# Optimization experiments

Measured on AMD Instinct MI355X. Metric: run time of the kernel, lower is better.

Reference implementation:

```python
import jax, jax.numpy as jnp
import numpy as np

B, L, H, NH = 8, 384, 512, 8
DH = H // NH
MAX_SEQ_LEN = 384


def setup_inputs() -> dict:
    key = jax.random.key(0)
    ks = jax.random.split(key, 16)
    s = 0.02
    seq_len = jnp.concatenate([
        jnp.array([L], dtype=jnp.int32),
        jax.random.randint(ks[3], (B - 1,), L // 2, L + 1, dtype=jnp.int32),
    ])
    return {
        "key": jax.random.normal(ks[0], (B, L, H), jnp.float32),
        "query": jax.random.normal(ks[1], (B, L, H), jnp.float32),
        "value": jax.random.normal(ks[2], (B, L, H), jnp.float32),
        "seq_len": seq_len,
        "pe": jax.random.normal(ks[4], (2 * MAX_SEQ_LEN + 1, H), jnp.float32) * s,
        "Wk": jax.random.normal(ks[5], (H, H), jnp.float32) * s,
        "bk": jnp.zeros((H,), jnp.float32),
        "Wq": jax.random.normal(ks[6], (H, H), jnp.float32) * s,
        "bq": jnp.zeros((H,), jnp.float32),
        "Wv": jax.random.normal(ks[7], (H, H), jnp.float32) * s,
        "bv": jnp.zeros((H,), jnp.float32),
        "Wr": jax.random.normal(ks[8], (H, H), jnp.float32) * s,
        "br": jnp.zeros((H,), jnp.float32),
        "u_bias": jax.random.normal(ks[9], (NH, DH), jnp.float32) * s,
        "v_bias": jax.random.normal(ks[10], (NH, DH), jnp.float32) * s,
        "Wff": jax.random.normal(ks[11], (H, H), jnp.float32) * s,
        "bff": jnp.zeros((H,), jnp.float32),
    }


def reference(key, query, value, seq_len, pe, Wk, bk, Wq, bq, Wv, bv, Wr, br, u_bias, v_bias, Wff, bff):
    # relative distances: rel[i, j] = j - i, in [-(L-1), L-1]
    rel = jnp.arange(L)[None, :] - jnp.arange(L)[:, None]          # [L, L]
    rpe = pe[rel + MAX_SEQ_LEN]                                    # [L, L, H]

    k = (key @ Wk.T + bk).reshape(B, L, NH, DH)
    q = (query @ Wq.T + bq).reshape(B, L, NH, DH)
    v = (value @ Wv.T + bv).reshape(B, L, NH, DH)
    rpe = (rpe @ Wr.T + br).reshape(L, L, NH, DH)

    # Transformer-XL score terms
    A = jnp.einsum('bihd,bjhd->bhij', q, k)                        # content-content
    Bt = jnp.einsum('bihd,ijhd->bhij', q, rpe)                     # content-position
    C = jnp.einsum('hd,bjhd->bhj', u_bias, k)[:, :, None, :]       # global content bias
    Dt = jnp.einsum('hd,ijhd->hij', v_bias, rpe)[None]             # global position bias

    scores = (A + Bt + C + Dt) / jnp.sqrt(jnp.float32(DH))
    key_mask = jnp.arange(L)[None, :] < seq_len[:, None]           # [B, L]
    scores = jnp.where(key_mask[:, None, None, :], scores, -1e15)
    attn = jax.nn.softmax(scores, axis=-1)                         # [B, NH, L, L]

    out = jnp.einsum('bhij,bjhd->bihd', attn, v).reshape(B, L, H)
    return out @ Wff.T + bff
```

## Files before the change

kernel.cpp:

```cpp
#include <hip/hip_runtime.h>

#define B_  8
#define L_  384
#define H_  512
#define NH_ 8
#define DH_ 64
#define RRM 768

typedef short bf16x8 __attribute__((ext_vector_type(8)));
typedef float f32x4  __attribute__((ext_vector_type(4)));
typedef unsigned int u32;
typedef u32 u32x4 __attribute__((ext_vector_type(4)));
#define MFMA_BF16 __builtin_amdgcn_mfma_f32_16x16x32_bf16

static __device__ __forceinline__ unsigned short f2bf(float f) {
    unsigned u = __builtin_bit_cast(unsigned, f);
    u += 0x7fffu + ((u >> 16) & 1u);
    return (unsigned short)(u >> 16);
}
static __device__ __forceinline__ float bf2f(unsigned short s) {
    unsigned u = ((unsigned)s) << 16;
    return __builtin_bit_cast(float, u);
}
static __device__ __forceinline__ u32 pk2(float lo, float hi) {
    u32 r;
    asm("v_cvt_pk_bf16_f32 %0, %1, %2" : "=v"(r) : "v"(lo), "v"(hi));
    return r;
}
static __device__ __forceinline__ void glds16(const void* g, void* l) {
    __builtin_amdgcn_global_load_lds(
        (const __attribute__((address_space(1))) u32*)g,
        (__attribute__((address_space(3))) u32*)l, 16, 0, 0);
}

struct WCvtArgs { const float* src[5]; unsigned short* dst[5]; };
__global__ __launch_bounds__(256) void cvt_w(WCvtArgs a) {
    const int gid = blockIdx.x * 256 + threadIdx.x;
    const int m = gid >> 15;
    const int rem = gid & 32767;
    const int row = rem >> 6, c = rem & 63;
    const int kc = c >> 3, sjd = c & 7;
    const int sjs = sjd ^ (row & 7);
    const float* s = a.src[m] + row * 512 + kc * 64 + sjs * 8;
    const f32x4 v0 = *(const f32x4*)s;
    const f32x4 v1 = *(const f32x4*)(s + 4);
    u32x4 o;
    o[0] = pk2(v0[0], v0[1]);
    o[1] = pk2(v0[2], v0[3]);
    o[2] = pk2(v1[0], v1[1]);
    o[3] = pk2(v1[2], v1[3]);
    *(u32x4*)(a.dst[m] + row * 512 + kc * 64 + sjd * 8) = o;
}

template <bool IS_FF>
__global__ __launch_bounds__(256) void gemm_nt(
    const float* __restrict__ A0, const float* __restrict__ A1,
    const float* __restrict__ A2, const float* __restrict__ A3,
    const unsigned short* __restrict__ Abf,
    const unsigned short* __restrict__ W0, const unsigned short* __restrict__ W1,
    const unsigned short* __restrict__ W2, const unsigned short* __restrict__ W3,
    const unsigned short* __restrict__ W4,
    const float* __restrict__ b0, const float* __restrict__ b1,
    const float* __restrict__ b2, const float* __restrict__ b3,
    const float* __restrict__ b4,
    const float* __restrict__ ub, const float* __restrict__ vbias,
    unsigned short* __restrict__ qu, unsigned short* __restrict__ qv,
    unsigned short* __restrict__ kb, unsigned short* __restrict__ vT,
    unsigned short* __restrict__ rp, float* __restrict__ ff) {

    const int z = IS_FF ? 4 : blockIdx.z;
    if (!IS_FF && z == 3 && blockIdx.y >= 12) return;
    const float* Af   = z == 0 ? A0 : z == 1 ? A1 : z == 2 ? A2 : A3;
    const unsigned short* Wb =
        z == 0 ? W0 : z == 1 ? W1 : z == 2 ? W2 : z == 3 ? W3 : W4;
    const float* bias = z == 0 ? b0 : z == 1 ? b1 : z == 2 ? b2 : z == 3 ? b3 : b4;

    __shared__ __align__(16) unsigned short AsF[2 * 64 * 64];
    __shared__ __align__(16) unsigned short BsF[2 * 128 * 64];

    const int tid = threadIdx.x;
    const int w = tid >> 6, lane = tid & 63;
    const int quad = lane >> 4, lm = lane & 15;
    const int wr = (w & 1) * 32;
    const int wc = (w >> 1) * 64;

    const int sr = lane >> 3, sj = lane & 7;
    const size_t aoff = (size_t)(blockIdx.y * 64 + w * 16 + sr) * 512 + sj * 8;
    const unsigned short* gB =
        Wb + (size_t)(blockIdx.x * 128 + w * 32 + sr) * 512 + sj * 8;

    f32x4 la[2][2];
    bf16x8 lah[2];

    auto LOAD_A = [&](int kc) {
        #pragma unroll
        for (int t2 = 0; t2 < 2; ++t2) {
            if constexpr (IS_FF) {
                lah[t2] = *(const bf16x8*)(Abf + aoff + t2 * 8 * 512 + kc * 64);
            } else {
                const float* p = Af + aoff + t2 * 8 * 512 + kc * 64;
                la[t2][0] = *(const f32x4*)p;
                la[t2][1] = *(const f32x4*)(p + 4);
            }
        }
    };
    auto WRITE_A = [&](int buf) {
        #pragma unroll
        for (int t2 = 0; t2 < 2; ++t2) {
            const int off = buf * 4096 + (w * 16 + t2 * 8 + sr) * 64 + (sj ^ sr) * 8;
            if constexpr (IS_FF) {
                *(bf16x8*)&AsF[off] = lah[t2];
            } else {
                u32x4 pa;
                pa[0] = pk2(la[t2][0][0], la[t2][0][1]);
                pa[1] = pk2(la[t2][0][2], la[t2][0][3]);
                pa[2] = pk2(la[t2][1][0], la[t2][1][1]);
                pa[3] = pk2(la[t2][1][2], la[t2][1][3]);
                *(u32x4*)&AsF[off] = pa;
            }
        }
    };
    auto STAGE_B = [&](int kc, int buf) {
        #pragma unroll
        for (int t2 = 0; t2 < 4; ++t2) {
            int off = buf * 8192 + (w * 32 + t2 * 8) * 64;
            off = __builtin_amdgcn_readfirstlane(off);
            glds16(gB + t2 * 8 * 512 + kc * 64, &BsF[off]);
        }
    };

    f32x4 acc[2][4] = {};
    LOAD_A(0);
    STAGE_B(0, 0);
    for (int kc = 0; kc < 8; ++kc) {
        const int buf = kc & 1;
        WRITE_A(buf);
        __syncthreads();
        if (kc < 7) {
            LOAD_A(kc + 1);
            STAGE_B(kc + 1, buf ^ 1);
        }
        const int ba = buf * 4096, bb = buf * 8192;
        #pragma unroll
        for (int ks = 0; ks < 2; ++ks) {
            const int s = (((ks * 4 + quad) ^ (lm & 7))) * 8;
            bf16x8 a0 = *(const bf16x8*)&AsF[ba + (wr + lm) * 64 + s];
            bf16x8 a1 = *(const bf16x8*)&AsF[ba + (wr + 16 + lm) * 64 + s];
            bf16x8 w0 = *(const bf16x8*)&BsF[bb + (wc + lm) * 64 + s];
            bf16x8 w1 = *(const bf16x8*)&BsF[bb + (wc + 16 + lm) * 64 + s];
            bf16x8 w2 = *(const bf16x8*)&BsF[bb + (wc + 32 + lm) * 64 + s];
            bf16x8 w3 = *(const bf16x8*)&BsF[bb + (wc + 48 + lm) * 64 + s];
            acc[0][0] = MFMA_BF16(a0, w0, acc[0][0], 0, 0, 0);
            acc[0][1] = MFMA_BF16(a0, w1, acc[0][1], 0, 0, 0);
            acc[0][2] = MFMA_BF16(a0, w2, acc[0][2], 0, 0, 0);
            acc[0][3] = MFMA_BF16(a0, w3, acc[0][3], 0, 0, 0);
            acc[1][0] = MFMA_BF16(a1, w0, acc[1][0], 0, 0, 0);
            acc[1][1] = MFMA_BF16(a1, w1, acc[1][1], 0, 0, 0);
            acc[1][2] = MFMA_BF16(a1, w2, acc[1][2], 0, 0, 0);
            acc[1][3] = MFMA_BF16(a1, w3, acc[1][3], 0, 0, 0);
        }
    }

    #pragma unroll
    for (int si = 0; si < 2; ++si) {
        #pragma unroll
        for (int sj2 = 0; sj2 < 4; ++sj2) {
            #pragma unroll
            for (int reg = 0; reg < 4; ++reg) {
                const int r = blockIdx.y * 64 + wr + si * 16 + quad * 4 + reg;
                const int c = blockIdx.x * 128 + wc + sj2 * 16 + lm;
                const float val = acc[si][sj2][reg] + bias[c];
                if (IS_FF) {
                    ff[r * 512 + c] = val;
                } else if (z == 0) {
                    const int bb2 = r / L_, ii = r - bb2 * L_;
                    const int h = c >> 6, d = c & 63;
                    const int idx = ((bb2 * NH_ + h) * L_ + ii) * DH_ + d;
                    qu[idx] = f2bf((val + ub[c]) * 0.125f);
                    qv[idx] = f2bf((val + vbias[c]) * 0.125f);
                } else if (z == 1) {
                    const int bb2 = r / L_, ii = r - bb2 * L_;
                    const int h = c >> 6, d = c & 63;
                    kb[((bb2 * NH_ + h) * L_ + ii) * DH_ + d] = f2bf(val);
                } else if (z == 2) {
                    const int bb2 = r / L_, ii = r - bb2 * L_;
                    const int h = c >> 6, d = c & 63;
                    vT[((bb2 * NH_ + h) * DH_ + d) * L_ + ii] = f2bf(val);
                } else {
                    rp[r * 512 + c] = f2bf(val);
                }
            }
        }
    }
}

#define BTSTR 424
__global__ __launch_bounds__(256) void attn_fused(
    const unsigned short* __restrict__ qu, const unsigned short* __restrict__ qv,
    const unsigned short* __restrict__ kbf, const unsigned short* __restrict__ vT,
    const unsigned short* __restrict__ rp, const int* __restrict__ seq_len,
    unsigned short* __restrict__ Obf) {
    __shared__ __align__(16) unsigned short BtP[32 * BTSTR];
    __shared__ float mx_red[32][2];
    __shared__ float sm_red[32][2];
    const int lane = threadIdx.x & 63, wv = threadIdx.x >> 6;
    const int quad = lane >> 4, lm = lane & 15;
    const int bh = blockIdx.y, b = bh >> 3, h = bh & 7;
    const int i0 = blockIdx.x * 32;
    const int sl = seq_len[b];
    const int msub = wv & 1, nh = wv >> 1;
    const int m_lo = 353 - i0;
    const int i_fr = i0 + msub * 16 + lm;

    {
        const unsigned short* qvr = qv + (size_t)(bh * L_ + i_fr) * DH_;
        const bf16x8 av0 = *(const bf16x8*)(qvr + quad * 8);
        const bf16x8 av1 = *(const bf16x8*)(qvr + 32 + quad * 8);
        #pragma unroll
        for (int ns = 0; ns < 13; ++ns) {
            const int ntl = nh * 208 + ns * 16;
            if (ntl <= sl + 30) {
                const int n = ntl + lm;
                const unsigned short* rrow = rp + (size_t)(m_lo + n) * 512 + h * 64;
                f32x4 bacc = {};
                bacc = MFMA_BF16(av0, *(const bf16x8*)(rrow + quad * 8), bacc, 0, 0, 0);
                bacc = MFMA_BF16(av1, *(const bf16x8*)(rrow + 32 + quad * 8), bacc, 0, 0, 0);
                #pragma unroll
                for (int reg = 0; reg < 4; ++reg) {
                    const int il = msub * 16 + quad * 4 + reg;
                    BtP[il * BTSTR + n] = f2bf(bacc[reg]);
                }
            }
        }
    }
    const unsigned short* qur = qu + (size_t)(bh * L_ + i_fr) * DH_;
    const bf16x8 au0 = *(const bf16x8*)(qur + quad * 8);
    const bf16x8 au1 = *(const bf16x8*)(qur + 32 + quad * 8);
    __syncthreads();

    f32x4 sc[12];
    #pragma unroll
    for (int ns = 0; ns < 12; ++ns) {
        const int jt = nh * 192 + ns * 16;
        if (jt < sl) {
            const unsigned short* krow = kbf + (size_t)(bh * L_ + jt + lm) * DH_;
            f32x4 a = {};
            a = MFMA_BF16(au0, *(const bf16x8*)(krow + quad * 8), a, 0, 0, 0);
            a = MFMA_BF16(au1, *(const bf16x8*)(krow + 32 + quad * 8), a, 0, 0, 0);
            sc[ns] = a;
        } else {
            sc[ns] = f32x4{-1e30f, -1e30f, -1e30f, -1e30f};
        }
    }
    const int jbase = nh * 192 + lm;
    #pragma unroll
    for (int ns = 0; ns < 12; ++ns) {
        const int j = jbase + ns * 16;
        #pragma unroll
        for (int reg = 0; reg < 4; ++reg) {
            const int il = msub * 16 + quad * 4 + reg;
            float val = -1e30f;
            if (j < sl) val = sc[ns][reg] + bf2f(BtP[il * BTSTR + (j - il + 31)]);
            sc[ns][reg] = val;
        }
    }

    const int il0 = msub * 16 + quad * 4;
    float mx4[4], sm4[4], inv4[4];
    #pragma unroll
    for (int reg = 0; reg < 4; ++reg) {
        float m = sc[0][reg];
        #pragma unroll
        for (int ns = 1; ns < 12; ++ns) m = fmaxf(m, sc[ns][reg]);
        #pragma unroll
        for (int o = 1; o < 16; o <<= 1) m = fmaxf(m, __shfl_xor(m, o));
        mx4[reg] = m;
    }
    if (lm == 0) {
        #pragma unroll
        for (int reg = 0; reg < 4; ++reg) mx_red[il0 + reg][nh] = mx4[reg];
    }
    __syncthreads();
    #pragma unroll
    for (int reg = 0; reg < 4; ++reg)
        mx4[reg] = fmaxf(mx_red[il0 + reg][0], mx_red[il0 + reg][1]);
    #pragma unroll
    for (int reg = 0; reg < 4; ++reg) sm4[reg] = 0.f;
    #pragma unroll
    for (int ns = 0; ns < 12; ++ns) {
        #pragma unroll
        for (int reg = 0; reg < 4; ++reg) {
            const float e = __expf(sc[ns][reg] - mx4[reg]);
            sc[ns][reg] = e;
            sm4[reg] += e;
        }
    }
    #pragma unroll
    for (int reg = 0; reg < 4; ++reg) {
        float s = sm4[reg];
        #pragma unroll
        for (int o = 1; o < 16; o <<= 1) s += __shfl_xor(s, o);
        sm4[reg] = s;
    }
    if (lm == 0) {
        #pragma unroll
        for (int reg = 0; reg < 4; ++reg) sm_red[il0 + reg][nh] = sm4[reg];
    }
    __syncthreads();
    #pragma unroll
    for (int reg = 0; reg < 4; ++reg)
        inv4[reg] = 1.f / (sm_red[il0 + reg][0] + sm_red[il0 + reg][1]);

    #pragma unroll
    for (int ns = 0; ns < 12; ++ns) {
        const int j = jbase + ns * 16;
        #pragma unroll
        for (int reg = 0; reg < 4; ++reg)
            BtP[(il0 + reg) * BTSTR + j] = f2bf(sc[ns][reg] * inv4[reg]);
    }
    __syncthreads();

    {
        const int pr = msub * 16 + lm;
        const int nkc = (sl + 31) >> 5;
        f32x4 oacc[2] = {};
        for (int kc = 0; kc < nkc; ++kc) {
            const bf16x8 af = *(const bf16x8*)&BtP[pr * BTSTR + kc * 32 + quad * 8];
            #pragma unroll
            for (int t = 0; t < 2; ++t) {
                const int n = nh * 32 + t * 16 + lm;
                const unsigned short* vrow = vT + (size_t)(bh * DH_ + n) * L_ + kc * 32 + quad * 8;
                oacc[t] = MFMA_BF16(af, *(const bf16x8*)(vrow), oacc[t], 0, 0, 0);
            }
        }
        #pragma unroll
        for (int t = 0; t < 2; ++t) {
            #pragma unroll
            for (int reg = 0; reg < 4; ++reg) {
                const int i = i0 + msub * 16 + quad * 4 + reg;
                const int d = nh * 32 + t * 16 + lm;
                Obf[(size_t)(b * L_ + i) * H_ + h * DH_ + d] = f2bf(oacc[t][reg]);
            }
        }
    }
}

extern "C" void kernel_launch(void* const* d_in, const int* in_sizes, int n_in,
                              void* d_out, int out_size, void* d_ws, size_t ws_size,
                              hipStream_t stream) {
    const float* key    = (const float*)d_in[0];
    const float* query  = (const float*)d_in[1];
    const float* value  = (const float*)d_in[2];
    const int*   seqlen = (const int*)d_in[3];
    const float* pe     = (const float*)d_in[4];
    const float* Wk     = (const float*)d_in[5];
    const float* bk     = (const float*)d_in[6];
    const float* Wq     = (const float*)d_in[7];
    const float* bq     = (const float*)d_in[8];
    const float* Wv     = (const float*)d_in[9];
    const float* bv     = (const float*)d_in[10];
    const float* Wr     = (const float*)d_in[11];
    const float* br     = (const float*)d_in[12];
    const float* u_bias = (const float*)d_in[13];
    const float* v_bias = (const float*)d_in[14];
    const float* Wff    = (const float*)d_in[15];
    const float* bff    = (const float*)d_in[16];

    const size_t nTok = (size_t)B_ * L_ * H_;
    const size_t nPe  = (size_t)RRM * H_;
    const size_t nW   = (size_t)H_ * H_;
    unsigned short* p  = (unsigned short*)d_ws;
    unsigned short* qu   = p; p += nTok;
    unsigned short* qv   = p; p += nTok;
    unsigned short* kb   = p; p += nTok;
    unsigned short* vT   = p; p += nTok;
    unsigned short* rp   = p; p += nPe + 512;
    unsigned short* Obf  = p; p += nTok;
    unsigned short* Wqb  = p; p += nW;
    unsigned short* Wkb  = p; p += nW;
    unsigned short* Wvb  = p; p += nW;
    unsigned short* Wrb  = p; p += nW;
    unsigned short* Wffb = p; p += nW;

    WCvtArgs wa;
    wa.src[0] = Wq;  wa.dst[0] = Wqb;
    wa.src[1] = Wk;  wa.dst[1] = Wkb;
    wa.src[2] = Wv;  wa.dst[2] = Wvb;
    wa.src[3] = Wr;  wa.dst[3] = Wrb;
    wa.src[4] = Wff; wa.dst[4] = Wffb;
    cvt_w<<<640, 256, 0, stream>>>(wa);

    gemm_nt<false><<<dim3(4, 48, 4), 256, 0, stream>>>(
         query, key, value, pe,  nullptr,
         Wqb, Wkb, Wvb, Wrb, nullptr,
         bq, bk, bv, br, nullptr,
         u_bias, v_bias,
         qu, qv, kb, vT, rp,
         nullptr);

    attn_fused<<<dim3(L_ / 32, B_ * NH_), 256, 0, stream>>>(
        qu, qv, kb, vT, rp, seqlen, Obf);

    gemm_nt<true><<<dim3(4, 48, 1), 256, 0, stream>>>(
         nullptr, nullptr, nullptr, nullptr,  Obf,
         nullptr, nullptr, nullptr, nullptr, Wffb,
         nullptr, nullptr, nullptr, nullptr, bff,
         nullptr, nullptr,
         nullptr, nullptr, nullptr, nullptr, nullptr,
         (float*)d_out);
}
```

Measured before the change: 157.3 us.

## Double M-tile of projection GEMM to 128 rows and restructure staging pipeline

The QKV/R projection GEMM now uses a 128-row A tile (four 16-row MFMA sub-tiles per wave) and launches half as many row blocks. This improves weight reuse per block and cuts block count. The FF GEMM keeps its 64-row tile. The pipeline also changes: B is staged into the current buffer just before the barrier, and a second barrier is added at the end of each k-step. This removes the earlier prefetch overlap of B with compute, and the larger tile raises register and LDS use.

```diff
diff --git a/kernel.cpp b/kernel.cpp
--- a/kernel.cpp
+++ b/kernel.cpp
@@ -68,33 +68,36 @@
     unsigned short* __restrict__ kb, unsigned short* __restrict__ vT,
     unsigned short* __restrict__ rp, float* __restrict__ ff) {
 
+    constexpr int SI = IS_FF ? 2 : 4;
+    constexpr int MT = SI * 32;
+
     const int z = IS_FF ? 4 : blockIdx.z;
-    if (!IS_FF && z == 3 && blockIdx.y >= 12) return;
+    if (!IS_FF && z == 3 && blockIdx.y >= (RRM / MT)) return;
     const float* Af   = z == 0 ? A0 : z == 1 ? A1 : z == 2 ? A2 : A3;
     const unsigned short* Wb =
         z == 0 ? W0 : z == 1 ? W1 : z == 2 ? W2 : z == 3 ? W3 : W4;
     const float* bias = z == 0 ? b0 : z == 1 ? b1 : z == 2 ? b2 : z == 3 ? b3 : b4;
 
-    __shared__ __align__(16) unsigned short AsF[2 * 64 * 64];
+    __shared__ __align__(16) unsigned short AsF[2 * MT * 64];
     __shared__ __align__(16) unsigned short BsF[2 * 128 * 64];
 
     const int tid = threadIdx.x;
     const int w = tid >> 6, lane = tid & 63;
     const int quad = lane >> 4, lm = lane & 15;
-    const int wr = (w & 1) * 32;
+    const int wr = (w & 1) * (SI * 16);
     const int wc = (w >> 1) * 64;
 
     const int sr = lane >> 3, sj = lane & 7;
-    const size_t aoff = (size_t)(blockIdx.y * 64 + w * 16 + sr) * 512 + sj * 8;
+    const size_t aoff = (size_t)(blockIdx.y * MT + w * (SI * 8) + sr) * 512 + sj * 8;
     const unsigned short* gB =
         Wb + (size_t)(blockIdx.x * 128 + w * 32 + sr) * 512 + sj * 8;
 
-    f32x4 la[2][2];
-    bf16x8 lah[2];
+    f32x4 la[SI][2];
+    bf16x8 lah[SI];
 
     auto LOAD_A = [&](int kc) {
         #pragma unroll
-        for (int t2 = 0; t2 < 2; ++t2) {
+        for (int t2 = 0; t2 < SI; ++t2) {
             if constexpr (IS_FF) {
                 lah[t2] = *(const bf16x8*)(Abf + aoff + t2 * 8 * 512 + kc * 64);
             } else {
@@ -106,8 +109,9 @@
     };
     auto WRITE_A = [&](int buf) {
         #pragma unroll
-        for (int t2 = 0; t2 < 2; ++t2) {
-            const int off = buf * 4096 + (w * 16 + t2 * 8 + sr) * 64 + (sj ^ sr) * 8;
+        for (int t2 = 0; t2 < SI; ++t2) {
+            const int off = buf * (MT * 64)
+                          + (w * (SI * 8) + t2 * 8 + sr) * 64 + (sj ^ sr) * 8;
             if constexpr (IS_FF) {
                 *(bf16x8*)&AsF[off] = lah[t2];
             } else {
@@ -129,45 +133,44 @@
         }
     };
 
-    f32x4 acc[2][4] = {};
+    f32x4 acc[SI][4] = {};
     LOAD_A(0);
-    STAGE_B(0, 0);
     for (int kc = 0; kc < 8; ++kc) {
         const int buf = kc & 1;
         WRITE_A(buf);
+        STAGE_B(kc, buf);
+        if (kc < 7) LOAD_A(kc + 1);
         __syncthreads();
-        if (kc < 7) {
-            LOAD_A(kc + 1);
-            STAGE_B(kc + 1, buf ^ 1);
-        }
-        const int ba = buf * 4096, bb = buf * 8192;
+        const int ba = buf * (MT * 64), bb = buf * 8192;
         #pragma unroll
         for (int ks = 0; ks < 2; ++ks) {
             const int s = (((ks * 4 + quad) ^ (lm & 7))) * 8;
-            bf16x8 a0 = *(const bf16x8*)&AsF[ba + (wr + lm) * 64 + s];
-            bf16x8 a1 = *(const bf16x8*)&AsF[ba + (wr + 16 + lm) * 64 + s];
+            bf16x8 av[SI];
+            #pragma unroll
+            for (int si = 0; si < SI; ++si)
+                av[si] = *(const bf16x8*)&AsF[ba + (wr + si * 16 + lm) * 64 + s];
             bf16x8 w0 = *(const bf16x8*)&BsF[bb + (wc + lm) * 64 + s];
             bf16x8 w1 = *(const bf16x8*)&BsF[bb + (wc + 16 + lm) * 64 + s];
             bf16x8 w2 = *(const bf16x8*)&BsF[bb + (wc + 32 + lm) * 64 + s];
             bf16x8 w3 = *(const bf16x8*)&BsF[bb + (wc + 48 + lm) * 64 + s];
-            acc[0][0] = MFMA_BF16(a0, w0, acc[0][0], 0, 0, 0);
-            acc[0][1] = MFMA_BF16(a0, w1, acc[0][1], 0, 0, 0);
-            acc[0][2] = MFMA_BF16(a0, w2, acc[0][2], 0, 0, 0);
-            acc[0][3] = MFMA_BF16(a0, w3, acc[0][3], 0, 0, 0);
-            acc[1][0] = MFMA_BF16(a1, w0, acc[1][0], 0, 0, 0);
-            acc[1][1] = MFMA_BF16(a1, w1, acc[1][1], 0, 0, 0);
-            acc[1][2] = MFMA_BF16(a1, w2, acc[1][2], 0, 0, 0);
-            acc[1][3] = MFMA_BF16(a1, w3, acc[1][3], 0, 0, 0);
-        }
-    }
-
-    #pragma unroll
-    for (int si = 0; si < 2; ++si) {
+            #pragma unroll
+            for (int si = 0; si < SI; ++si) {
+                acc[si][0] = MFMA_BF16(av[si], w0, acc[si][0], 0, 0, 0);
+                acc[si][1] = MFMA_BF16(av[si], w1, acc[si][1], 0, 0, 0);
+                acc[si][2] = MFMA_BF16(av[si], w2, acc[si][2], 0, 0, 0);
+                acc[si][3] = MFMA_BF16(av[si], w3, acc[si][3], 0, 0, 0);
+            }
+        }
+        __syncthreads();
+    }
+
+    #pragma unroll
+    for (int si = 0; si < SI; ++si) {
         #pragma unroll
         for (int sj2 = 0; sj2 < 4; ++sj2) {
             #pragma unroll
             for (int reg = 0; reg < 4; ++reg) {
-                const int r = blockIdx.y * 64 + wr + si * 16 + quad * 4 + reg;
+                const int r = blockIdx.y * MT + wr + si * 16 + quad * 4 + reg;
                 const int c = blockIdx.x * 128 + wc + sj2 * 16 + lm;
                 const float val = acc[si][sj2][reg] + bias[c];
                 if (IS_FF) {
@@ -390,7 +393,7 @@
     wa.src[4] = Wff; wa.dst[4] = Wffb;
     cvt_w<<<640, 256, 0, stream>>>(wa);
 
-    gemm_nt<false><<<dim3(4, 48, 4), 256, 0, stream>>>(
+    gemm_nt<false><<<dim3(4, 24, 4), 256, 0, stream>>>(
          query, key, value, pe,  nullptr,
          Wqb, Wkb, Wvb, Wrb, nullptr,
          bq, bk, bv, br, nullptr,
```

New measurement: 163.2 us. +3.7%, slower.
